# Optimization experiments

Hardware: AMD Instinct MI355X
Metric: run time of the kernel (lower is better)

Reference implementation:

```python
import jax, jax.numpy as jnp
import numpy as np

FRAME_LEN = 512
HOP_LEN = 128
FFT_SIZE = 512
N_SAMPLES = -1  # TF slice [:, :-1] drops the final sample
B, FRAMES, BINS = 16, 4000, FFT_SIZE // 2 + 1


def _inverse_window():
    # tf.signal.hann_window (periodic): 0.5 - 0.5*cos(2*pi*n/N)
    n = jnp.arange(FRAME_LEN, dtype=jnp.float32)
    win = 0.5 - 0.5 * jnp.cos(2.0 * np.pi * n / FRAME_LEN)
    # tf.signal.inverse_stft_window_fn: divide by overlap-added squared window
    denom = win * win
    overlaps = -(-FRAME_LEN // HOP_LEN)  # ceil div
    denom = jnp.pad(denom, (0, overlaps * HOP_LEN - FRAME_LEN))
    denom = denom.reshape(overlaps, HOP_LEN).sum(axis=0)  # [HOP_LEN]
    denom = jnp.tile(denom, overlaps)[:FRAME_LEN]
    return win / denom


def setup_inputs() -> dict:
    key = jax.random.key(0)
    k1, k2 = jax.random.split(key)
    return {
        "stft_real": jax.random.normal(k1, (B, FRAMES, BINS), dtype=jnp.float32),
        "stft_imag": jax.random.normal(k2, (B, FRAMES, BINS), dtype=jnp.float32),
    }


def reference(stft_real, stft_imag):
    stfts = jax.lax.complex(stft_real, stft_imag)  # [B, F, BINS] complex64
    # per-frame inverse real FFT, truncate to frame_length
    frames = jnp.fft.irfft(stfts, n=FFT_SIZE, axis=-1)[..., :FRAME_LEN]  # [B, F, L] float32
    frames = frames * _inverse_window()  # broadcast window over [B, F, L]
    out_len = (FRAMES - 1) * HOP_LEN + FRAME_LEN
    # overlap-add via vectorized scatter-accumulate
    idx = jnp.arange(FRAMES)[:, None] * HOP_LEN + jnp.arange(FRAME_LEN)[None, :]  # [F, L]
    sig = jnp.zeros((B, out_len), dtype=jnp.float32).at[:, idx].add(frames)
    return sig[:, :N_SAMPLES]
```

## Files before the change

### kernel.cpp

```cpp
#include <hip/hip_runtime.h>
#include <math.h>

#define HOP       128
#define NBINS     257
#define NFRAMES   4000
#define NB        16
#define OUT_LEN   512383
#define CPR       8
#define RPB       501
#define NCHUNK    4003
#define PB        320

__device__ __forceinline__ float2 cmul(float2 a, float2 b) {
    return make_float2(a.x*b.x - a.y*b.y, a.x*b.y + a.y*b.x);
}

__device__ __forceinline__ void dft4(const float2* x, float2* y) {
    const float s0r=x[0].x+x[2].x, s0i=x[0].y+x[2].y;
    const float d0r=x[0].x-x[2].x, d0i=x[0].y-x[2].y;
    const float s1r=x[1].x+x[3].x, s1i=x[1].y+x[3].y;
    const float d1r=x[1].x-x[3].x, d1i=x[1].y-x[3].y;
    y[0]=make_float2(s0r+s1r, s0i+s1i);
    y[2]=make_float2(s0r-s1r, s0i-s1i);
    y[1]=make_float2(d0r-d1i, d0i+d1r);
    y[3]=make_float2(d0r+d1i, d0i-d1r);
}

__global__ __launch_bounds__(256)
void istft_pk_kernel(const float* __restrict__ re,
                     const float* __restrict__ im,
                     float* __restrict__ out)
{
    __shared__ float2 pbuf[4][PB];

    const int tid = threadIdx.x;
    const int wv  = tid >> 6;
    const int l   = tid & 63;
    float2* P = pbuf[wv];

    const int rid = blockIdx.x * 4 + wv;
    const int b   = rid / RPB;
    const int rr  = rid - b * RPB;
    const int c0  = rr * CPR;
    const int fend = min(c0 + CPR - 1, NCHUNK - 1);

    const float* __restrict__ reb = re + (size_t)b * NFRAMES * NBINS;
    const float* __restrict__ imb = im + (size_t)b * NFRAMES * NBINS;
    float* __restrict__ outb = out + (size_t)b * OUT_LEN;

    const float TWO_PI = 6.2831853071795864f;
    float2 ctw[4];
    {
        float s, c; __sincosf(TWO_PI * (float)l * (1.0f/512.0f), &s, &c);
        const float R = 0.70710678118654752f;
        ctw[0] = make_float2(c, s);
        #pragma unroll
        for (int j = 1; j < 4; ++j) {
            const float cn = (c - s) * R, sn = (s + c) * R;
            c = cn; s = sn; ctw[j] = make_float2(c, s);
        }
    }
    float2 w1, w2, w3;
    { float s, c; __sincosf(TWO_PI * (float)l * (1.0f/256.0f), &s, &c);
      w1 = make_float2(c, s); w2 = cmul(w1, w1); w3 = cmul(w2, w1); }
    float2 b1, b2, b3;
    { float s, c; __sincosf(TWO_PI * (float)(l & 15) * (1.0f/64.0f), &s, &c);
      b1 = make_float2(c, s); b2 = cmul(b1, b1); b3 = cmul(b2, b1); }
    float2 q1, q2, q3;
    { float s, c; __sincosf(TWO_PI * (float)(l & 3) * (1.0f/16.0f), &s, &c);
      q1 = make_float2(c, s); q2 = cmul(q1, q1); q3 = cmul(q2, q1); }
    float wwx[4], wwy[4];
    {
        const float S = 6.5104166667e-4f;
        float sx, cx; __sincosf(TWO_PI * (float)(2*l) * (1.0f/512.0f), &sx, &cx);
        wwx[0]=S*(1.0f-cx); wwx[1]=S*(1.0f+sx); wwx[2]=S*(1.0f+cx); wwx[3]=S*(1.0f-sx);
        float sy, cy; __sincosf(TWO_PI * (float)(2*l+1) * (1.0f/512.0f), &sy, &cy);
        wwy[0]=S*(1.0f-cy); wwy[1]=S*(1.0f+sy); wwy[2]=S*(1.0f+cy); wwy[3]=S*(1.0f-sy);
    }
    const int a1w = l;
    const int a1r = (l & 15) + 64 * (l >> 4);
    const int a2w = (l & 15) + 20 * (l >> 4);
    const int a2r = (l & 3) + 20 * ((l >> 2) & 3) + 80 * (l >> 4);
    const int a3w = ((l >> 2) & 3) + 4 * (l >> 4) + 20 * (l & 3);
    const int a3r = (l & 3) + 4 * ((l >> 2) & 3) + 80 * (l >> 4);

    float accx[4], accy[4];
    #pragma unroll
    for (int o = 0; o < 4; ++o) { accx[o] = 0.0f; accy[o] = 0.0f; }

    for (int f = c0 - 3; f <= fend; ++f) {
        if (f >= 0 && f < NFRAMES) {
            const float* __restrict__ rb = reb + (size_t)f * NBINS;
            const float* __restrict__ ib = imb + (size_t)f * NBINS;

            float2 Cv[4];
            #pragma unroll
            for (int j = 0; j < 4; ++j) {
                const int k  = l + 64*j;
                const int km = 256 - k;
                float ydr = rb[k],  ydi = ib[k];
                float ymr = rb[km], ymi = ib[km];
                if (j == 0) {
                    const bool z = (l == 0);
                    ydi = z ? 0.0f : ydi;
                    ymi = z ? 0.0f : ymi;
                }
                const float er  = ydr + ymr, ei  = ydi - ymi;
                const float fr2 = ydr - ymr, fi2 = ydi + ymi;
                const float gr = ctw[j].x*fr2 - ctw[j].y*fi2;
                const float gi = ctw[j].x*fi2 + ctw[j].y*fr2;
                Cv[j] = make_float2(er - gi, ei + gr);
            }

            float2 A[4], G[4];
            dft4(Cv, A);
            A[1] = cmul(A[1], w1); A[2] = cmul(A[2], w2); A[3] = cmul(A[3], w3);
            P[a1w] = A[0]; P[a1w+64] = A[1]; P[a1w+128] = A[2]; P[a1w+192] = A[3];
            __builtin_amdgcn_wave_barrier();
            G[0] = P[a1r]; G[1] = P[a1r+16]; G[2] = P[a1r+32]; G[3] = P[a1r+48];
            __builtin_amdgcn_wave_barrier();

            dft4(G, A);
            A[1] = cmul(A[1], b1); A[2] = cmul(A[2], b2); A[3] = cmul(A[3], b3);
            P[a2w] = A[0]; P[a2w+80] = A[1]; P[a2w+160] = A[2]; P[a2w+240] = A[3];
            __builtin_amdgcn_wave_barrier();
            G[0] = P[a2r]; G[1] = P[a2r+4]; G[2] = P[a2r+8]; G[3] = P[a2r+12];
            __builtin_amdgcn_wave_barrier();

            dft4(G, A);
            A[1] = cmul(A[1], q1); A[2] = cmul(A[2], q2); A[3] = cmul(A[3], q3);
            P[a3w] = A[0]; P[a3w+80] = A[1]; P[a3w+160] = A[2]; P[a3w+240] = A[3];
            __builtin_amdgcn_wave_barrier();
            G[0] = P[a3r]; G[1] = P[a3r+20]; G[2] = P[a3r+40]; G[3] = P[a3r+60];
            __builtin_amdgcn_wave_barrier();

            dft4(G, A);

            #pragma unroll
            for (int o = 0; o < 4; ++o) {
                accx[o] += A[o].x * wwx[o];
                accy[o] += A[o].y * wwy[o];
            }
        }

        if (f >= c0) {
            const int s0 = f * HOP + 2*l;
            outb[s0] = accx[0];
            const int s1 = s0 + 1;
            if (s1 < OUT_LEN) outb[s1] = accy[0];
        }

        #pragma unroll
        for (int o = 0; o < 3; ++o) { accx[o] = accx[o+1]; accy[o] = accy[o+1]; }
        accx[3] = 0.0f; accy[3] = 0.0f;
    }
}

extern "C" void kernel_launch(void* const* d_in, const int* in_sizes, int n_in,
                              void* d_out, int out_size, void* d_ws, size_t ws_size,
                              hipStream_t stream) {
    (void)in_sizes; (void)n_in; (void)d_ws; (void)ws_size; (void)out_size;
    const float* re = (const float*)d_in[0];
    const float* im = (const float*)d_in[1];
    float* out = (float*)d_out;

    const int nblocks = (NB * RPB) / 4;
    istft_pk_kernel<<<dim3(nblocks), dim3(256), 0, stream>>>(re, im, out);
}
```

Before: 175.8 us.

## Software-pipeline frame loads and FFT stages with double-buffered LDS

Restructures the per-frame loop so the global loads for the next frame are issued before the remaining FFT stages of the current frame run. The first FFT stage writes into an alternating LDS buffer. The intent is to hide global memory latency behind compute. It removes the wave barriers and doubles LDS use per block, which adds register pressure and relies on implicit ordering within a wave.

```diff
diff --git a/kernel.cpp b/kernel.cpp
--- a/kernel.cpp
+++ b/kernel.cpp
@@ -9,7 +9,7 @@
 #define CPR       8
 #define RPB       501
 #define NCHUNK    4003
-#define PB        320
+#define PBF       320
 
 __device__ __forceinline__ float2 cmul(float2 a, float2 b) {
     return make_float2(a.x*b.x - a.y*b.y, a.x*b.y + a.y*b.x);
@@ -27,16 +27,18 @@
 }
 
 __global__ __launch_bounds__(256)
-void istft_pk_kernel(const float* __restrict__ re,
-                     const float* __restrict__ im,
-                     float* __restrict__ out)
+void istft_pk2_kernel(const float* __restrict__ re,
+                      const float* __restrict__ im,
+                      float* __restrict__ out)
 {
-    __shared__ float2 pbuf[4][PB];
+    __shared__ float2 bufA[4][PBF];
+    __shared__ float2 bufB[4][PBF];
 
     const int tid = threadIdx.x;
     const int wv  = tid >> 6;
     const int l   = tid & 63;
-    float2* P = pbuf[wv];
+    float2* PA = bufA[wv];
+    float2* PBp = bufB[wv];
 
     const int rid = blockIdx.x * 4 + wv;
     const int b   = rid / RPB;
@@ -88,71 +90,83 @@
     #pragma unroll
     for (int o = 0; o < 4; ++o) { accx[o] = 0.0f; accy[o] = 0.0f; }
 
-    for (int f = c0 - 3; f <= fend; ++f) {
+    float dr[4], di[4], mr4[4], mi4[4];
+
+    auto issue_loads = [&](int fq) {
+        const int fc = min(max(fq, 0), NFRAMES - 1);
+        const float* __restrict__ rb = reb + (size_t)fc * NBINS;
+        const float* __restrict__ ib = imb + (size_t)fc * NBINS;
+        #pragma unroll
+        for (int j = 0; j < 4; ++j) {
+            const int k = l + 64*j, km = 256 - k;
+            dr[j]  = rb[k];  di[j]  = ib[k];
+            mr4[j] = rb[km]; mi4[j] = ib[km];
+        }
+    };
+
+    auto stage1 = [&](float2* __restrict__ P) {
+        float2 Cv[4];
+        #pragma unroll
+        for (int j = 0; j < 4; ++j) {
+            float ydr = dr[j], ydi = di[j], ymr = mr4[j], ymi = mi4[j];
+            if (j == 0) {
+                const bool z = (l == 0);
+                ydi = z ? 0.0f : ydi;
+                ymi = z ? 0.0f : ymi;
+            }
+            const float er  = ydr + ymr, ei  = ydi - ymi;
+            const float fr2 = ydr - ymr, fi2 = ydi + ymi;
+            const float gr = ctw[j].x*fr2 - ctw[j].y*fi2;
+            const float gi = ctw[j].x*fi2 + ctw[j].y*fr2;
+            Cv[j] = make_float2(er - gi, ei + gr);
+        }
+        float2 A[4];
+        dft4(Cv, A);
+        A[1] = cmul(A[1], w1); A[2] = cmul(A[2], w2); A[3] = cmul(A[3], w3);
+        P[a1w] = A[0]; P[a1w+64] = A[1]; P[a1w+128] = A[2]; P[a1w+192] = A[3];
+    };
+
+    auto stages234 = [&](float2* __restrict__ P, int f) {
+        float2 A[4], G[4];
+        G[0] = P[a1r]; G[1] = P[a1r+16]; G[2] = P[a1r+32]; G[3] = P[a1r+48];
+        dft4(G, A);
+        A[1] = cmul(A[1], b1); A[2] = cmul(A[2], b2); A[3] = cmul(A[3], b3);
+        P[a2w] = A[0]; P[a2w+80] = A[1]; P[a2w+160] = A[2]; P[a2w+240] = A[3];
+        G[0] = P[a2r]; G[1] = P[a2r+4]; G[2] = P[a2r+8]; G[3] = P[a2r+12];
+        dft4(G, A);
+        A[1] = cmul(A[1], q1); A[2] = cmul(A[2], q2); A[3] = cmul(A[3], q3);
+        P[a3w] = A[0]; P[a3w+80] = A[1]; P[a3w+160] = A[2]; P[a3w+240] = A[3];
+        G[0] = P[a3r]; G[1] = P[a3r+20]; G[2] = P[a3r+40]; G[3] = P[a3r+60];
+        dft4(G, A);
         if (f >= 0 && f < NFRAMES) {
-            const float* __restrict__ rb = reb + (size_t)f * NBINS;
-            const float* __restrict__ ib = imb + (size_t)f * NBINS;
-
-            float2 Cv[4];
-            #pragma unroll
-            for (int j = 0; j < 4; ++j) {
-                const int k  = l + 64*j;
-                const int km = 256 - k;
-                float ydr = rb[k],  ydi = ib[k];
-                float ymr = rb[km], ymi = ib[km];
-                if (j == 0) {
-                    const bool z = (l == 0);
-                    ydi = z ? 0.0f : ydi;
-                    ymi = z ? 0.0f : ymi;
-                }
-                const float er  = ydr + ymr, ei  = ydi - ymi;
-                const float fr2 = ydr - ymr, fi2 = ydi + ymi;
-                const float gr = ctw[j].x*fr2 - ctw[j].y*fi2;
-                const float gi = ctw[j].x*fi2 + ctw[j].y*fr2;
-                Cv[j] = make_float2(er - gi, ei + gr);
-            }
-
-            float2 A[4], G[4];
-            dft4(Cv, A);
-            A[1] = cmul(A[1], w1); A[2] = cmul(A[2], w2); A[3] = cmul(A[3], w3);
-            P[a1w] = A[0]; P[a1w+64] = A[1]; P[a1w+128] = A[2]; P[a1w+192] = A[3];
-            __builtin_amdgcn_wave_barrier();
-            G[0] = P[a1r]; G[1] = P[a1r+16]; G[2] = P[a1r+32]; G[3] = P[a1r+48];
-            __builtin_amdgcn_wave_barrier();
-
-            dft4(G, A);
-            A[1] = cmul(A[1], b1); A[2] = cmul(A[2], b2); A[3] = cmul(A[3], b3);
-            P[a2w] = A[0]; P[a2w+80] = A[1]; P[a2w+160] = A[2]; P[a2w+240] = A[3];
-            __builtin_amdgcn_wave_barrier();
-            G[0] = P[a2r]; G[1] = P[a2r+4]; G[2] = P[a2r+8]; G[3] = P[a2r+12];
-            __builtin_amdgcn_wave_barrier();
-
-            dft4(G, A);
-            A[1] = cmul(A[1], q1); A[2] = cmul(A[2], q2); A[3] = cmul(A[3], q3);
-            P[a3w] = A[0]; P[a3w+80] = A[1]; P[a3w+160] = A[2]; P[a3w+240] = A[3];
-            __builtin_amdgcn_wave_barrier();
-            G[0] = P[a3r]; G[1] = P[a3r+20]; G[2] = P[a3r+40]; G[3] = P[a3r+60];
-            __builtin_amdgcn_wave_barrier();
-
-            dft4(G, A);
-
             #pragma unroll
             for (int o = 0; o < 4; ++o) {
                 accx[o] += A[o].x * wwx[o];
                 accy[o] += A[o].y * wwy[o];
             }
         }
-
         if (f >= c0) {
             const int s0 = f * HOP + 2*l;
             outb[s0] = accx[0];
             const int s1 = s0 + 1;
             if (s1 < OUT_LEN) outb[s1] = accy[0];
         }
-
         #pragma unroll
         for (int o = 0; o < 3; ++o) { accx[o] = accx[o+1]; accy[o] = accy[o+1]; }
         accx[3] = 0.0f; accy[3] = 0.0f;
+    };
+
+    issue_loads(c0 - 3);
+    stage1(PA);
+    for (int f = c0 - 3; f <= fend; f += 2) {
+        issue_loads(f + 1);
+        stages234(PA, f);
+        stage1(PBp);
+        if (f + 1 <= fend) {
+            issue_loads(f + 2);
+            stages234(PBp, f + 1);
+            stage1(PA);
+        }
     }
 }
 
@@ -165,5 +179,5 @@
     float* out = (float*)d_out;
 
     const int nblocks = (NB * RPB) / 4;
-    istft_pk_kernel<<<dim3(nblocks), dim3(256), 0, stream>>>(re, im, out);
+    istft_pk2_kernel<<<dim3(nblocks), dim3(256), 0, stream>>>(re, im, out);
 }
```

New measurement: 174.9 us. No clear change (-0.5%).
